# Kernel tuning notes

Measured on AMD Instinct MI355X. Metric: run time of the kernel, lower is better.

## Reference

```python
import jax, jax.numpy as jnp
import numpy as np

N = 10000
E = 320000
D = 256
EPS = 1e-5

def layer_norm(x, g, b):
    mu = jnp.mean(x, axis=-1, keepdims=True)
    var = jnp.mean(jnp.square(x - mu), axis=-1, keepdims=True)
    return (x - mu) * jax.lax.rsqrt(var + EPS) * g + b

def linear(x, w, b):
    # w: [in, out]
    return x @ w + b

def setup_inputs() -> dict:
    key = jax.random.key(0)
    ks = jax.random.split(key, 20)
    s = 1.0 / np.sqrt(D)
    inp = {
        'x': jax.random.normal(ks[0], (N, D), jnp.float32),
        'edge_index': jax.random.randint(ks[1], (2, E), 0, N, jnp.int64),
        'edge_weight': jax.random.normal(ks[2], (E,), jnp.float32),
        'wq': jax.random.normal(ks[3], (D, D), jnp.float32) * s,
        'bq': jnp.zeros((D,), jnp.float32),
        'wk': jax.random.normal(ks[4], (D, D), jnp.float32) * s,
        'bk': jnp.zeros((D,), jnp.float32),
        'wv': jax.random.normal(ks[5], (D, D), jnp.float32) * s,
        'bv': jnp.zeros((D,), jnp.float32),
        'ws': jax.random.normal(ks[6], (D, D), jnp.float32) * s,
        'bs': jnp.zeros((D,), jnp.float32),
        'we': jax.random.normal(ks[7], (1, 1), jnp.float32),
        'be': jnp.zeros((1,), jnp.float32),
        'g1': jnp.ones((D,), jnp.float32),
        'b1': jnp.zeros((D,), jnp.float32),
        'g2': jnp.ones((D,), jnp.float32),
        'b2': jnp.zeros((D,), jnp.float32),
        'w_ff1': jax.random.normal(ks[8], (D, 2 * D), jnp.float32) * s,
        'b_ff1': jnp.zeros((2 * D,), jnp.float32),
        'w_ff2': jax.random.normal(ks[9], (2 * D, D), jnp.float32) * (1.0 / np.sqrt(2 * D)),
        'b_ff2': jnp.zeros((D,), jnp.float32),
    }
    return inp

def reference(x, edge_index, edge_weight, wq, bq, wk, bk, wv, bv, ws, bs, we, be,
              g1, b1, g2, b2, w_ff1, b_ff1, w_ff2, b_ff2):
    n = x.shape[0]
    scale = x.shape[-1] ** (-0.5)
    q = linear(x, wq, bq)
    k = linear(x, wk, bk)
    v = linear(x, wv, bv)
    src, dst = edge_index[0], edge_index[1]
    # per-edge attention scores: dot(q[dst], k[src]) * scale
    scores = jnp.sum(q[dst] * k[src], axis=-1) * scale
    scores = scores + (edge_weight[:, None] @ we + be)[:, 0]
    # two-pass segment softmax over dst
    seg_max = jax.ops.segment_max(scores, dst, num_segments=n)
    exp_s = jnp.exp(scores - seg_max[dst])
    denom = jax.ops.segment_sum(exp_s, dst, num_segments=n)
    attn = exp_s / jnp.maximum(denom[dst], 1e-12)
    # scatter-add weighted messages
    message = v[src] * attn[:, None]  # [E, D]
    out = jax.ops.segment_sum(message, dst, num_segments=n)
    x = layer_norm(x + out + linear(x, ws, bs), g1, b1)
    ffn = linear(jax.nn.gelu(linear(x, w_ff1, b_ff1)), w_ff2, b_ff2)
    x = layer_norm(x + ffn, g2, b2)
    return x
```

## Files before the change

### kernel.cpp

```cpp
#include <hip/hip_runtime.h>
#include <math.h>

#define N_NODES 10000
#define N_EDGES 320000
#define DIM 256
#define BCAP 128

typedef __attribute__((ext_vector_type(8))) short bf16x8;
typedef __attribute__((ext_vector_type(4))) float fx4;


__device__ __forceinline__ float gelu_tanh(float x) {
  const float k0 = 0.7978845608028654f;
  float x3 = x * x * x;
  return 0.5f * x * (1.0f + tanhf(k0 * (x + 0.044715f * x3)));
}

__device__ __forceinline__ unsigned short f2bf(float f) {
  unsigned u = __float_as_uint(f);
  unsigned r = 0x7FFFu + ((u >> 16) & 1u);
  return (unsigned short)((u + r) >> 16);
}

__device__ __forceinline__ float bf_lo(unsigned u) { return __uint_as_float(u << 16); }
__device__ __forceinline__ float bf_hi(unsigned u) { return __uint_as_float(u & 0xFFFF0000u); }


#define SEG_QKVS 262144
#define SEG_FF1 131072
#define SEG_FF2 131072
#define SEG_BIAS 1024
#define SEG_CONV 320000
#define SEG_ZCNT 10000
#define PREP_TOTAL (SEG_QKVS + SEG_FF1 + SEG_FF2 + SEG_BIAS + SEG_CONV + SEG_ZCNT)

__global__ __launch_bounds__(256) void prep_all_kernel(
    const float* __restrict__ wq, const float* __restrict__ wk,
    const float* __restrict__ wv, const float* __restrict__ ws,
    const float* __restrict__ bq, const float* __restrict__ bk,
    const float* __restrict__ bv, const float* __restrict__ bs,
    const float* __restrict__ wff1, const float* __restrict__ wff2,
    const float* __restrict__ x,
    unsigned short* __restrict__ wt_qkvs, float* __restrict__ bias_qkvs,
    unsigned short* __restrict__ wt_ff1, unsigned short* __restrict__ wt_ff2,
    unsigned short* __restrict__ xb, unsigned* __restrict__ cnt) {
  int id = blockIdx.x * 256 + threadIdx.x;
  if (id < SEG_QKVS) {
    const int n = id >> 8, k = id & 255;
    const float* w = (n < 256) ? wq : (n < 512) ? wk : (n < 768) ? wv : ws;
    wt_qkvs[id] = f2bf(w[k * 256 + (n & 255)]);
    return;
  }
  id -= SEG_QKVS;
  if (id < SEG_FF1) {
    const int n = id >> 8, k = id & 255;
    wt_ff1[id] = f2bf(wff1[k * 512 + n]);
    return;
  }
  id -= SEG_FF1;
  if (id < SEG_FF2) {
    const int n = id >> 9, k = id & 511;
    wt_ff2[id] = f2bf(wff2[k * 256 + n]);
    return;
  }
  id -= SEG_FF2;
  if (id < SEG_BIAS) {
    bias_qkvs[id] = (id < 256) ? bq[id] : (id < 512) ? bk[id & 255]
                    : (id < 768) ? bv[id & 255] : bs[id & 255];
    return;
  }
  id -= SEG_BIAS;
  if (id < SEG_CONV) {
    const int base = id * 8;
    float4 a = *(const float4*)(x + base);
    float4 b = *(const float4*)(x + base + 4);
    unsigned short h[8] = {f2bf(a.x), f2bf(a.y), f2bf(a.z), f2bf(a.w),
                           f2bf(b.x), f2bf(b.y), f2bf(b.z), f2bf(b.w)};
    *(uint4*)(xb + base) = *(const uint4*)h;
    return;
  }
  id -= SEG_CONV;
  if (id < SEG_ZCNT) cnt[id] = 0u;
}

template <int GELU, int WF32, int WB16, int SPLIT>
__global__ __launch_bounds__(256) void mfma_gemm(
    const unsigned short* __restrict__ A, int lda,
    const unsigned short* __restrict__ Bt,
    const float* __restrict__ bias,
    const float* __restrict__ xres,
    float* __restrict__ C, int ldc,
    unsigned short* __restrict__ Cb, int ldcb,
    int M, int K,
    const int* __restrict__ ei, const float* __restrict__ ew,
    const float* __restrict__ we, const float* __restrict__ be,
    unsigned* __restrict__ cnt, uint2* __restrict__ es_csr) {
  __shared__ unsigned short As[64 * 64];
  __shared__ unsigned short Bs[64 * 64];
  const int tid = threadIdx.x;

  if (SPLIT) {
    const int bid = blockIdx.y * gridDim.x + blockIdx.x;
    const int stride = gridDim.x * gridDim.y * 256;
    const float wes = we[0], bes = be[0];
    for (int e = bid * 256 + tid; e < N_EDGES; e += stride) {
      const int dst = ei[N_EDGES + e];
      const unsigned pos = atomicAdd(cnt + dst, 1u);
      uint2 es;
      es.x = (unsigned)ei[e];
      es.y = __float_as_uint(ew[e] * wes + bes);
      es_csr[(size_t)dst * BCAP + pos] = es;
    }
  }

  const int l = tid & 63;
  const int wid = tid >> 6;
  const int wrow = (wid & 1) * 32;
  const int wcol = (wid >> 1) * 32;
  const int bm = blockIdx.y * 64;
  const int bn = blockIdx.x * 64;

  fx4 acc[2][2];
#pragma unroll
  for (int i = 0; i < 2; i++)
#pragma unroll
    for (int j = 0; j < 2; j++) acc[i][j] = (fx4)(0.0f);

  for (int kb = 0; kb < K; kb += 64) {
    __syncthreads();
#pragma unroll
    for (int i = 0; i < 2; i++) {
      const int id = i * 256 + tid;
      const int row = id >> 3;
      const int cc = id & 7;
      const int dsto = row * 128 + ((cc << 4) ^ ((row & 7) << 4));
      uint4 av = make_uint4(0, 0, 0, 0);
      const int gr = bm + row;
      if (gr < M) av = *(const uint4*)(A + (size_t)gr * lda + kb + cc * 8);
      *(uint4*)((char*)As + dsto) = av;
    }
#pragma unroll
    for (int i = 0; i < 2; i++) {
      const int id = i * 256 + tid;
      const int row = id >> 3;
      const int cc = id & 7;
      const int dsto = row * 128 + ((cc << 4) ^ ((row & 7) << 4));
      uint4 bv = *(const uint4*)(Bt + (size_t)(bn + row) * K + kb + cc * 8);
      *(uint4*)((char*)Bs + dsto) = bv;
    }
    __syncthreads();
#pragma unroll
    for (int kk = 0; kk < 2; kk++) {
      const int kbyte = (kk * 64 + ((l >> 4) << 4)) ^ ((l & 7) << 4);
      bf16x8 af[2], bg[2];
#pragma unroll
      for (int f = 0; f < 2; f++) {
        const int ar = wrow + f * 16 + (l & 15);
        af[f] = *(const bf16x8*)((const char*)As + ar * 128 + kbyte);
        const int br = wcol + f * 16 + (l & 15);
        bg[f] = *(const bf16x8*)((const char*)Bs + br * 128 + kbyte);
      }
#pragma unroll
      for (int fr = 0; fr < 2; fr++)
#pragma unroll
        for (int fc = 0; fc < 2; fc++)
          acc[fr][fc] = __builtin_amdgcn_mfma_f32_16x16x32_bf16(
              af[fr], bg[fc], acc[fr][fc], 0, 0, 0);
    }
  }

#pragma unroll
  for (int fr = 0; fr < 2; fr++) {
    const int m0 = bm + wrow + fr * 16 + ((l >> 4) << 2);
#pragma unroll
    for (int fc = 0; fc < 2; fc++) {
      const int n = bn + wcol + fc * 16 + (l & 15);
      const float bn_ = bias[n];
      fx4 v = acc[fr][fc];
#pragma unroll
      for (int r = 0; r < 4; r++) {
        const int row = m0 + r;
        if (row < M) {
          float o = v[r] + bn_;
          if (GELU) o = gelu_tanh(o);
          if (SPLIT) {
            const int seg = n >> 8, nn = n & 255;
            if (seg == 3)
              C[(size_t)row * 256 + nn] = o + xres[(size_t)row * 256 + nn];
            else
              Cb[(size_t)seg * (N_NODES * DIM) + (size_t)row * 256 + nn] = f2bf(o);
          } else {
            if (WF32) C[(size_t)row * ldc + n] = o;
            if (WB16) Cb[(size_t)row * ldcb + n] = f2bf(o);
          }
        }
      }
    }
  }
}

__global__ __launch_bounds__(64) void agg_fused_kernel(
    const unsigned* __restrict__ cnt, const uint2* __restrict__ es_csr,
    const unsigned short* __restrict__ qb,
    const unsigned short* __restrict__ kb, const unsigned short* __restrict__ vb,
    const float* __restrict__ sbuf,
    const float* __restrict__ g, const float* __restrict__ b,
    float* __restrict__ out, unsigned short* __restrict__ outb) {
  const int node = blockIdx.x;
  const int lane = threadIdx.x;
  const int grp = lane >> 4;
  const int t = lane & 15;
  const int start = node * BCAP;
  const int deg = min((int)cnt[node], BCAP);
  const int end = start + deg;

  const uint4 qA = *(const uint4*)(qb + (size_t)node * 256 + t * 16);
  const uint4 qB = *(const uint4*)(qb + (size_t)node * 256 + t * 16 + 8);
  float qf[16];
  qf[0] = bf_lo(qA.x);  qf[1] = bf_hi(qA.x);
  qf[2] = bf_lo(qA.y);  qf[3] = bf_hi(qA.y);
  qf[4] = bf_lo(qA.z);  qf[5] = bf_hi(qA.z);
  qf[6] = bf_lo(qA.w);  qf[7] = bf_hi(qA.w);
  qf[8] = bf_lo(qB.x);  qf[9] = bf_hi(qB.x);
  qf[10] = bf_lo(qB.y); qf[11] = bf_hi(qB.y);
  qf[12] = bf_lo(qB.z); qf[13] = bf_hi(qB.z);
  qf[14] = bf_lo(qB.w); qf[15] = bf_hi(qB.w);

  float m = -3.4e38f, dsum = 0.f;
  float a0 = 0.f, a1 = 0.f, a2 = 0.f, a3 = 0.f;

  int ea = start + grp * 2;
  int eb_ = ea + 1;
  bool va = ea < end, vbd = eb_ < end;
  int sa = 0, sb = 0;
  float ba = 0.f, bb = 0.f;
  if (va) { const uint2 es = es_csr[ea]; sa = (int)es.x; ba = __uint_as_float(es.y); }
  if (vbd) { const uint2 es = es_csr[eb_]; sb = (int)es.x; bb = __uint_as_float(es.y); }
  uint4 kAa = *(const uint4*)(kb + (size_t)sa * 256 + t * 16);
  uint4 kBa = *(const uint4*)(kb + (size_t)sa * 256 + t * 16 + 8);
  uint4 kAb = *(const uint4*)(kb + (size_t)sb * 256 + t * 16);
  uint4 kBb = *(const uint4*)(kb + (size_t)sb * 256 + t * 16 + 8);

  for (int base = start; base < end; base += 8) {
    const int s0 = __shfl(sa, 0), s1 = __shfl(sa, 16);
    const int s2 = __shfl(sa, 32), s3 = __shfl(sa, 48);
    const int s4 = __shfl(sb, 0), s5 = __shfl(sb, 16);
    const int s6 = __shfl(sb, 32), s7 = __shfl(sb, 48);
    const uint2 v0 = *(const uint2*)(vb + (size_t)s0 * 256 + lane * 4);
    const uint2 v1 = *(const uint2*)(vb + (size_t)s1 * 256 + lane * 4);
    const uint2 v2 = *(const uint2*)(vb + (size_t)s2 * 256 + lane * 4);
    const uint2 v3 = *(const uint2*)(vb + (size_t)s3 * 256 + lane * 4);
    const uint2 v4 = *(const uint2*)(vb + (size_t)s4 * 256 + lane * 4);
    const uint2 v5 = *(const uint2*)(vb + (size_t)s5 * 256 + lane * 4);
    const uint2 v6 = *(const uint2*)(vb + (size_t)s6 * 256 + lane * 4);
    const uint2 v7 = *(const uint2*)(vb + (size_t)s7 * 256 + lane * 4);

    const int na = base + 8 + grp * 2;
    const int nb = na + 1;
    const bool va_n = na < end, vb_n = nb < end;
    int sa_n = 0, sb_n = 0;
    float ba_n = 0.f, bb_n = 0.f;
    if (va_n) { const uint2 es = es_csr[na]; sa_n = (int)es.x; ba_n = __uint_as_float(es.y); }
    if (vb_n) { const uint2 es = es_csr[nb]; sb_n = (int)es.x; bb_n = __uint_as_float(es.y); }

    float da = qf[0] * bf_lo(kAa.x);
    float db = qf[0] * bf_lo(kAb.x);
    da = fmaf(qf[1], bf_hi(kAa.x), da);  db = fmaf(qf[1], bf_hi(kAb.x), db);
    da = fmaf(qf[2], bf_lo(kAa.y), da);  db = fmaf(qf[2], bf_lo(kAb.y), db);
    da = fmaf(qf[3], bf_hi(kAa.y), da);  db = fmaf(qf[3], bf_hi(kAb.y), db);
    da = fmaf(qf[4], bf_lo(kAa.z), da);  db = fmaf(qf[4], bf_lo(kAb.z), db);
    da = fmaf(qf[5], bf_hi(kAa.z), da);  db = fmaf(qf[5], bf_hi(kAb.z), db);
    da = fmaf(qf[6], bf_lo(kAa.w), da);  db = fmaf(qf[6], bf_lo(kAb.w), db);
    da = fmaf(qf[7], bf_hi(kAa.w), da);  db = fmaf(qf[7], bf_hi(kAb.w), db);
    da = fmaf(qf[8], bf_lo(kBa.x), da);  db = fmaf(qf[8], bf_lo(kBb.x), db);
    da = fmaf(qf[9], bf_hi(kBa.x), da);  db = fmaf(qf[9], bf_hi(kBb.x), db);
    da = fmaf(qf[10], bf_lo(kBa.y), da); db = fmaf(qf[10], bf_lo(kBb.y), db);
    da = fmaf(qf[11], bf_hi(kBa.y), da); db = fmaf(qf[11], bf_hi(kBb.y), db);
    da = fmaf(qf[12], bf_lo(kBa.z), da); db = fmaf(qf[12], bf_lo(kBb.z), db);
    da = fmaf(qf[13], bf_hi(kBa.z), da); db = fmaf(qf[13], bf_hi(kBb.z), db);
    da = fmaf(qf[14], bf_lo(kBa.w), da); db = fmaf(qf[14], bf_lo(kBb.w), db);
    da = fmaf(qf[15], bf_hi(kBa.w), da); db = fmaf(qf[15], bf_hi(kBb.w), db);
    da += __shfl_xor(da, 1);  db += __shfl_xor(db, 1);
    da += __shfl_xor(da, 2);  db += __shfl_xor(db, 2);
    da += __shfl_xor(da, 4);  db += __shfl_xor(db, 4);
    da += __shfl_xor(da, 8);  db += __shfl_xor(db, 8);
    const float sca = va ? fmaf(da, 0.0625f, ba) : -3.4e38f;
    const float scb = vbd ? fmaf(db, 0.0625f, bb) : -3.4e38f;

    const uint4 kAa_n = *(const uint4*)(kb + (size_t)sa_n * 256 + t * 16);
    const uint4 kBa_n = *(const uint4*)(kb + (size_t)sa_n * 256 + t * 16 + 8);
    const uint4 kAb_n = *(const uint4*)(kb + (size_t)sb_n * 256 + t * 16);
    const uint4 kBb_n = *(const uint4*)(kb + (size_t)sb_n * 256 + t * 16 + 8);

    const float c0 = __shfl(sca, 0), c1 = __shfl(sca, 16);
    const float c2 = __shfl(sca, 32), c3 = __shfl(sca, 48);
    const float c4 = __shfl(scb, 0), c5 = __shfl(scb, 16);
    const float c6 = __shfl(scb, 32), c7 = __shfl(scb, 48);

    const float mx = fmaxf(fmaxf(fmaxf(c0, c1), fmaxf(c2, c3)),
                           fmaxf(fmaxf(c4, c5), fmaxf(c6, c7)));
    const float mn = fmaxf(m, mx);
    const float scale = __expf(m - mn);
    const float w0 = __expf(c0 - mn), w1 = __expf(c1 - mn);
    const float w2 = __expf(c2 - mn), w3 = __expf(c3 - mn);
    const float w4 = __expf(c4 - mn), w5 = __expf(c5 - mn);
    const float w6 = __expf(c6 - mn), w7 = __expf(c7 - mn);
    dsum = fmaf(dsum, scale, ((w0 + w1) + (w2 + w3)) + ((w4 + w5) + (w6 + w7)));

    float t0 = a0 * scale;
    t0 = fmaf(w0, bf_lo(v0.x), t0); t0 = fmaf(w1, bf_lo(v1.x), t0);
    t0 = fmaf(w2, bf_lo(v2.x), t0); t0 = fmaf(w3, bf_lo(v3.x), t0);
    t0 = fmaf(w4, bf_lo(v4.x), t0); t0 = fmaf(w5, bf_lo(v5.x), t0);
    t0 = fmaf(w6, bf_lo(v6.x), t0); t0 = fmaf(w7, bf_lo(v7.x), t0);
    a0 = t0;
    float t1 = a1 * scale;
    t1 = fmaf(w0, bf_hi(v0.x), t1); t1 = fmaf(w1, bf_hi(v1.x), t1);
    t1 = fmaf(w2, bf_hi(v2.x), t1); t1 = fmaf(w3, bf_hi(v3.x), t1);
    t1 = fmaf(w4, bf_hi(v4.x), t1); t1 = fmaf(w5, bf_hi(v5.x), t1);
    t1 = fmaf(w6, bf_hi(v6.x), t1); t1 = fmaf(w7, bf_hi(v7.x), t1);
    a1 = t1;
    float t2 = a2 * scale;
    t2 = fmaf(w0, bf_lo(v0.y), t2); t2 = fmaf(w1, bf_lo(v1.y), t2);
    t2 = fmaf(w2, bf_lo(v2.y), t2); t2 = fmaf(w3, bf_lo(v3.y), t2);
    t2 = fmaf(w4, bf_lo(v4.y), t2); t2 = fmaf(w5, bf_lo(v5.y), t2);
    t2 = fmaf(w6, bf_lo(v6.y), t2); t2 = fmaf(w7, bf_lo(v7.y), t2);
    a2 = t2;
    float t3 = a3 * scale;
    t3 = fmaf(w0, bf_hi(v0.y), t3); t3 = fmaf(w1, bf_hi(v1.y), t3);
    t3 = fmaf(w2, bf_hi(v2.y), t3); t3 = fmaf(w3, bf_hi(v3.y), t3);
    t3 = fmaf(w4, bf_hi(v4.y), t3); t3 = fmaf(w5, bf_hi(v5.y), t3);
    t3 = fmaf(w6, bf_hi(v6.y), t3); t3 = fmaf(w7, bf_hi(v7.y), t3);
    a3 = t3;
    m = mn;

    sa = sa_n; sb = sb_n;
    ba = ba_n; bb = bb_n;
    va = va_n; vbd = vb_n;
    kAa = kAa_n; kBa = kBa_n;
    kAb = kAb_n; kBb = kBb_n;
  }
  const float inv = 1.0f / fmaxf(dsum, 1e-12f);

  const float4 sv = *(const float4*)(sbuf + (size_t)node * 256 + lane * 4);
  float r0 = a0 * inv + sv.x;
  float r1 = a1 * inv + sv.y;
  float r2 = a2 * inv + sv.z;
  float r3 = a3 * inv + sv.w;

  float sum = r0 + r1 + r2 + r3;
#pragma unroll
  for (int off = 32; off > 0; off >>= 1) sum += __shfl_xor(sum, off);
  const float mu = sum * (1.0f / 256.0f);
  const float d0 = r0 - mu, d1 = r1 - mu, d2 = r2 - mu, d3 = r3 - mu;
  float vs = d0 * d0 + d1 * d1 + d2 * d2 + d3 * d3;
#pragma unroll
  for (int off = 32; off > 0; off >>= 1) vs += __shfl_xor(vs, off);
  const float rs = rsqrtf(vs * (1.0f / 256.0f) + 1e-5f);

  const float4 gv = *(const float4*)(g + lane * 4);
  const float4 bv = *(const float4*)(b + lane * 4);
  float4 o;
  o.x = d0 * rs * gv.x + bv.x;
  o.y = d1 * rs * gv.y + bv.y;
  o.z = d2 * rs * gv.z + bv.z;
  o.w = d3 * rs * gv.w + bv.w;
  *(float4*)(out + (size_t)node * 256 + lane * 4) = o;
  uint2 pk;
  pk.x = (unsigned)f2bf(o.x) | ((unsigned)f2bf(o.y) << 16);
  pk.y = (unsigned)f2bf(o.z) | ((unsigned)f2bf(o.w) << 16);
  *(uint2*)(outb + (size_t)node * 256 + lane * 4) = pk;
}


__global__ __launch_bounds__(256) void ln2_kernel(
    const float* __restrict__ x1, const float* __restrict__ y,
    const float* __restrict__ g, const float* __restrict__ b,
    float* __restrict__ out) {
  __shared__ float red[4];
  const int row = blockIdx.x;
  const int t = threadIdx.x;
  float v = x1[(size_t)row * 256 + t] + y[(size_t)row * 256 + t];
  float s = v;
#pragma unroll
  for (int off = 32; off > 0; off >>= 1) s += __shfl_xor(s, off);
  if ((t & 63) == 0) red[t >> 6] = s;
  __syncthreads();
  float tot = red[0] + red[1] + red[2] + red[3];
  __syncthreads();
  const float mu = tot * (1.0f / 256.0f);
  const float d = v - mu;
  float vs = d * d;
#pragma unroll
  for (int off = 32; off > 0; off >>= 1) vs += __shfl_xor(vs, off);
  if ((t & 63) == 0) red[t >> 6] = vs;
  __syncthreads();
  float vtot = red[0] + red[1] + red[2] + red[3];
  const float r = rsqrtf(vtot * (1.0f / 256.0f) + 1e-5f);
  out[(size_t)row * 256 + t] = d * r * g[t] + b[t];
}


extern "C" void kernel_launch(void* const* d_in, const int* in_sizes, int n_in,
                              void* d_out, int out_size, void* d_ws,
                              size_t ws_size, hipStream_t stream) {
  const float* x = (const float*)d_in[0];
  const int* ei = (const int*)d_in[1];
  const float* ew = (const float*)d_in[2];
  const float* wq = (const float*)d_in[3];
  const float* bq = (const float*)d_in[4];
  const float* wk = (const float*)d_in[5];
  const float* bk = (const float*)d_in[6];
  const float* wv = (const float*)d_in[7];
  const float* bv = (const float*)d_in[8];
  const float* wsm = (const float*)d_in[9];
  const float* bs = (const float*)d_in[10];
  const float* we = (const float*)d_in[11];
  const float* be = (const float*)d_in[12];
  const float* g1 = (const float*)d_in[13];
  const float* b1 = (const float*)d_in[14];
  const float* g2 = (const float*)d_in[15];
  const float* b2 = (const float*)d_in[16];
  const float* wff1 = (const float*)d_in[17];
  const float* bff1 = (const float*)d_in[18];
  const float* wff2 = (const float*)d_in[19];
  const float* bff2 = (const float*)d_in[20];
  float* out = (float*)d_out;

  unsigned short* qb = (unsigned short*)d_ws;
  unsigned short* kbp = qb + 2560000;
  unsigned short* vbp = qb + 5120000;
  float* sbuf = (float*)(qb + 7680000);
  uint2* es_csr = (uint2*)(sbuf + 2560000);
  unsigned* cnt = (unsigned*)(es_csr + (size_t)N_NODES * BCAP);
  float* x1 = (float*)(cnt + N_NODES);
  float* y = x1 + 2560000;
  unsigned short* x1b = (unsigned short*)(y + 2560000);
  unsigned short* h_b = x1b + 2560000;
  unsigned short* xb = h_b;
  unsigned short* wt_qkvs = h_b + 5120000;
  unsigned short* wt_ff1 = wt_qkvs + 262144;
  unsigned short* wt_ff2 = wt_ff1 + 131072;
  float* bias_qkvs = (float*)(wt_ff2 + 131072);

  dim3 blk(256);
  const int mb = (N_NODES + 63) / 64;

  prep_all_kernel<<<(PREP_TOTAL + 255) / 256, blk, 0, stream>>>(
      wq, wk, wv, wsm, bq, bk, bv, bs, wff1, wff2, x,
      wt_qkvs, bias_qkvs, wt_ff1, wt_ff2, xb, cnt);

  mfma_gemm<0, 0, 0, 1><<<dim3(16, mb), blk, 0, stream>>>(
      xb, 256, wt_qkvs, bias_qkvs, x, sbuf, 0, qb, 0, N_NODES, 256,
      ei, ew, we, be, cnt, es_csr);

  agg_fused_kernel<<<N_NODES, dim3(64), 0, stream>>>(
      cnt, es_csr, qb, kbp, vbp, sbuf, g1, b1, x1, x1b);

  mfma_gemm<1, 0, 1, 0><<<dim3(8, mb), blk, 0, stream>>>(
      x1b, 256, wt_ff1, bff1, nullptr, (float*)nullptr, 0, h_b, 512, N_NODES, 256,
      nullptr, nullptr, nullptr, nullptr, nullptr, nullptr);

  mfma_gemm<0, 1, 0, 0><<<dim3(4, mb), blk, 0, stream>>>(
      h_b, 512, wt_ff2, bff2, nullptr, y, 256, (unsigned short*)nullptr, 0, N_NODES, 512,
      nullptr, nullptr, nullptr, nullptr, nullptr, nullptr);

  ln2_kernel<<<N_NODES, blk, 0, stream>>>(x1, y, g2, b2, out);
}
```

Measured before the change: 136.3 us.

## Double-buffer GEMM tiles with direct global-to-LDS async loads

Replaces the register-staged global→LDS tile copy with __builtin_amdgcn_global_load_lds direct loads into a double-buffered 32KB LDS region, prefetching the next K tile while computing the current one. The XOR swizzle moves to the global source address, and the M bounds check on A rows is dropped. This aims to hide global-load latency and cut VGPR traffic. The risks are out-of-bounds reads for the last partial M tile and a reliance on manual vmcnt accounting.

```diff
diff --git a/kernel.cpp b/kernel.cpp
--- a/kernel.cpp
+++ b/kernel.cpp
@@ -8,6 +8,9 @@
 
 typedef __attribute__((ext_vector_type(8))) short bf16x8;
 typedef __attribute__((ext_vector_type(4))) float fx4;
+
+typedef __attribute__((address_space(3))) unsigned lds_u32;
+typedef __attribute__((address_space(1))) const unsigned gbl_u32;
 
 
 __device__ __forceinline__ float gelu_tanh(float x) {
@@ -95,8 +98,7 @@
     const int* __restrict__ ei, const float* __restrict__ ew,
     const float* __restrict__ we, const float* __restrict__ be,
     unsigned* __restrict__ cnt, uint2* __restrict__ es_csr) {
-  __shared__ unsigned short As[64 * 64];
-  __shared__ unsigned short Bs[64 * 64];
+  __shared__ char lds[32768];
   const int tid = threadIdx.x;
 
   if (SPLIT) {
@@ -126,29 +128,41 @@
 #pragma unroll
     for (int j = 0; j < 2; j++) acc[i][j] = (fx4)(0.0f);
 
+#define STAGE(BUFOFF, KB)                                                      \
+  {                                                                            \
+    _Pragma("unroll") for (int i = 0; i < 2; i++) {                            \
+      const int id = i * 256 + tid;                                            \
+      const int row = id >> 3;                                                 \
+      const int ccs = (id & 7) ^ (row & 7);                                    \
+      __builtin_amdgcn_global_load_lds(                                        \
+          (gbl_u32*)(A + (size_t)(bm + row) * lda + (KB) + ccs * 8),           \
+          (lds_u32*)(lds + (BUFOFF) + id * 16), 16, 0, 0);                     \
+    }                                                                          \
+    _Pragma("unroll") for (int i = 0; i < 2; i++) {                            \
+      const int id = i * 256 + tid;                                            \
+      const int row = id >> 3;                                                 \
+      const int ccs = (id & 7) ^ (row & 7);                                    \
+      __builtin_amdgcn_global_load_lds(                                        \
+          (gbl_u32*)(Bt + (size_t)(bn + row) * K + (KB) + ccs * 8),            \
+          (lds_u32*)(lds + (BUFOFF) + 8192 + id * 16), 16, 0, 0);              \
+    }                                                                          \
+  }
+
+  STAGE(0, 0);
+
+  unsigned cur = 0;
   for (int kb = 0; kb < K; kb += 64) {
-    __syncthreads();
-#pragma unroll
-    for (int i = 0; i < 2; i++) {
-      const int id = i * 256 + tid;
-      const int row = id >> 3;
-      const int cc = id & 7;
-      const int dsto = row * 128 + ((cc << 4) ^ ((row & 7) << 4));
-      uint4 av = make_uint4(0, 0, 0, 0);
-      const int gr = bm + row;
-      if (gr < M) av = *(const uint4*)(A + (size_t)gr * lda + kb + cc * 8);
-      *(uint4*)((char*)As + dsto) = av;
+    if (kb + 64 < K) {
+      STAGE((cur ^ 1) * 16384, kb + 64);
+      asm volatile("s_waitcnt vmcnt(4)" ::: "memory");
+    } else {
+      asm volatile("s_waitcnt vmcnt(0)" ::: "memory");
     }
-#pragma unroll
-    for (int i = 0; i < 2; i++) {
-      const int id = i * 256 + tid;
-      const int row = id >> 3;
-      const int cc = id & 7;
-      const int dsto = row * 128 + ((cc << 4) ^ ((row & 7) << 4));
-      uint4 bv = *(const uint4*)(Bt + (size_t)(bn + row) * K + kb + cc * 8);
-      *(uint4*)((char*)Bs + dsto) = bv;
-    }
-    __syncthreads();
+    __builtin_amdgcn_s_barrier();
+    __builtin_amdgcn_sched_barrier(0);
+
+    const char* As = lds + cur * 16384;
+    const char* Bs = As + 8192;
 #pragma unroll
     for (int kk = 0; kk < 2; kk++) {
       const int kbyte = (kk * 64 + ((l >> 4) << 4)) ^ ((l & 7) << 4);
@@ -156,9 +170,9 @@
 #pragma unroll
       for (int f = 0; f < 2; f++) {
         const int ar = wrow + f * 16 + (l & 15);
-        af[f] = *(const bf16x8*)((const char*)As + ar * 128 + kbyte);
+        af[f] = *(const bf16x8*)(As + ar * 128 + kbyte);
         const int br = wcol + f * 16 + (l & 15);
-        bg[f] = *(const bf16x8*)((const char*)Bs + br * 128 + kbyte);
+        bg[f] = *(const bf16x8*)(Bs + br * 128 + kbyte);
       }
 #pragma unroll
       for (int fr = 0; fr < 2; fr++)
@@ -167,7 +181,10 @@
           acc[fr][fc] = __builtin_amdgcn_mfma_f32_16x16x32_bf16(
               af[fr], bg[fc], acc[fr][fc], 0, 0, 0);
     }
-  }
+    __builtin_amdgcn_s_barrier();
+    cur ^= 1;
+  }
+#undef STAGE
 
 #pragma unroll
   for (int fr = 0; fr < 2; fr++) {
```

New measurement: 138.5 us. No clear change (+1.6%).
